# Kernel optimization log

Hardware: AMD Instinct MI355X
Metric: run time of the kernel (lower is better)

The kernel has to match this reference:

```python
import jax, jax.numpy as jnp
import numpy as np

D_MODEL = 1024
HEADS = 16
D_K = D_MODEL // HEADS
B, S = 2, 2048
NEG = -1000000000.0

def setup_inputs() -> dict:
    key = jax.random.key(0)
    ks = jax.random.split(key, 11)
    sc = 1.0 / np.sqrt(D_MODEL)
    inp = {
        'q': jax.random.normal(ks[0], (B, S, D_MODEL), jnp.float32),
        'k': jax.random.normal(ks[1], (B, S, D_MODEL), jnp.float32),
        'v': jax.random.normal(ks[2], (B, S, D_MODEL), jnp.float32),
        'mask': jnp.tril(jnp.ones((S, S), jnp.int32))[None, None],  # causal [1,1,S,S]
        'wq_w': jax.random.normal(ks[3], (D_MODEL, D_MODEL), jnp.float32) * sc,
        'wq_b': jax.random.normal(ks[4], (D_MODEL,), jnp.float32) * 0.02,
        'wk_w': jax.random.normal(ks[5], (D_MODEL, D_MODEL), jnp.float32) * sc,
        'wk_b': jax.random.normal(ks[6], (D_MODEL,), jnp.float32) * 0.02,
        'wv_w': jax.random.normal(ks[7], (D_MODEL, D_MODEL), jnp.float32) * sc,
        'wv_b': jax.random.normal(ks[8], (D_MODEL,), jnp.float32) * 0.02,
        'wo_w': jax.random.normal(ks[9], (D_MODEL, D_MODEL), jnp.float32) * sc,
        'wo_b': jax.random.normal(ks[10], (D_MODEL,), jnp.float32) * 0.02,
    }
    return inp

def reference(q, k, v, mask, wq_w, wq_b, wk_w, wk_b, wv_w, wv_b, wo_w, wo_b):
    b, s, _ = q.shape
    # projections (torch Linear: x @ W^T + b)
    Q = (q @ wq_w.T + wq_b).reshape(b, s, HEADS, D_K).transpose(0, 2, 1, 3)  # [B,H,S,Dk]
    K = (k @ wk_w.T + wk_b).reshape(b, s, HEADS, D_K).transpose(0, 2, 1, 3)
    V = (v @ wv_w.T + wv_b).reshape(b, s, HEADS, D_K).transpose(0, 2, 1, 3)
    scores = jnp.einsum('bhqd,bhkd->bhqk', Q, K) / jnp.sqrt(jnp.float32(D_K))
    scores = jnp.where(mask == 0, NEG, scores)
    p = jax.nn.softmax(scores, axis=-1)  # dropout=0.0 -> identity
    x = jnp.einsum('bhqk,bhkd->bhqd', p, V)
    x = x.transpose(0, 2, 1, 3).reshape(b, s, D_MODEL)
    return x @ wo_w.T + wo_b
```

## Files before the change

### kernel.cpp

```cpp
#include <hip/hip_runtime.h>

typedef unsigned short u16;
typedef __attribute__((ext_vector_type(8))) short bf16x8;
typedef __attribute__((ext_vector_type(4))) float f32x4;

#define SEQ 2048
#define DMODEL 1024

__device__ __forceinline__ u16 f2bf(float f) {
    union { float f; unsigned u; } x; x.f = f;
    unsigned r = x.u + 0x7fffu + ((x.u >> 16) & 1u);
    return (u16)(r >> 16);
}

__device__ __forceinline__ u16 f2bf_trunc(float f) {
    union { float f; unsigned u; } x; x.f = f;
    return (u16)(x.u >> 16);
}

__device__ __forceinline__ f32x4 mfma16(bf16x8 a, bf16x8 b, f32x4 c) {
    return __builtin_amdgcn_mfma_f32_16x16x32_bf16(a, b, c, 0, 0, 0);
}

__device__ __forceinline__ void gld16(const u16* g, u16* l) {
    __builtin_amdgcn_global_load_lds(
        (__attribute__((address_space(1))) const void*)g,
        (__attribute__((address_space(3))) void*)l, 16, 0, 0);
}

struct CvtArgs {
    const float* src[7];
    u16* dst[7];
    int n4[7];
};

__global__ __launch_bounds__(256) void cvt_kernel(CvtArgs a) {
    const int id = blockIdx.y;
    const int i = blockIdx.x * 256 + threadIdx.x;
    if (i >= a.n4[id]) return;
    float4 f = ((const float4*)a.src[id])[i];
    ushort4 u;
    u.x = f2bf(f.x); u.y = f2bf(f.y); u.z = f2bf(f.z); u.w = f2bf(f.w);
    ((ushort4*)a.dst[id])[i] = u;
}

__global__ __launch_bounds__(256) void gemm_qkv(
    const u16* __restrict__ Xq, const u16* __restrict__ Xk, const u16* __restrict__ Xv,
    const u16* __restrict__ Wq, const u16* __restrict__ Wk, const u16* __restrict__ Wv,
    const float* __restrict__ bq, const float* __restrict__ bk, const float* __restrict__ bv,
    u16* __restrict__ Qb, u16* __restrict__ Kb, u16* __restrict__ Vb)
{
    const int z = blockIdx.z;
    const u16* X = (z == 0) ? Xq : (z == 1) ? Xk : Xv;
    const u16* W = (z == 0) ? Wq : (z == 1) ? Wk : Wv;
    const float* bias = (z == 0) ? bq : (z == 1) ? bk : bv;

    __shared__ u16 As[128 * 32];
    __shared__ u16 Bs[128 * 32];

    const int tid = threadIdx.x;
    const int bm = blockIdx.y * 128, bn = blockIdx.x * 128;
    const int lane = tid & 63, w = tid >> 6;
    const int wm = (w >> 1) * 64, wn = (w & 1) * 64;
    const int r = lane & 15, qd = lane >> 4;

    const int cb0 = w * 64;
    const int cb1 = 256 + w * 64;
    const int c0 = cb0 + lane, c1 = cb1 + lane;
    const int r0 = c0 >> 2, o0 = (c0 & 3) * 8;
    const int r1 = c1 >> 2, o1 = (c1 & 3) * 8;

    f32x4 acc[4][4];
    #pragma unroll
    for (int i = 0; i < 4; ++i)
        #pragma unroll
        for (int j = 0; j < 4; ++j)
            acc[i][j] = (f32x4){0.f, 0.f, 0.f, 0.f};

    for (int kk = 0; kk < 1024; kk += 32) {
        __syncthreads();
        gld16(X + (size_t)(bm + r0) * 1024 + kk + o0, As + cb0 * 8);
        gld16(X + (size_t)(bm + r1) * 1024 + kk + o1, As + cb1 * 8);
        gld16(W + (size_t)(bn + r0) * 1024 + kk + o0, Bs + cb0 * 8);
        gld16(W + (size_t)(bn + r1) * 1024 + kk + o1, Bs + cb1 * 8);
        __syncthreads();

        bf16x8 aF[4], bF[4];
        #pragma unroll
        for (int i = 0; i < 4; ++i)
            aF[i] = *(const bf16x8*)(As + (wm + i * 16 + r) * 32 + qd * 8);
        #pragma unroll
        for (int j = 0; j < 4; ++j)
            bF[j] = *(const bf16x8*)(Bs + (wn + j * 16 + r) * 32 + qd * 8);
        #pragma unroll
        for (int i = 0; i < 4; ++i)
            #pragma unroll
            for (int j = 0; j < 4; ++j)
                acc[i][j] = mfma16(aF[i], bF[j], acc[i][j]);
    }

    const float scale = (z == 0) ? 0.125f : 1.0f;
    #pragma unroll
    for (int j = 0; j < 4; ++j) {
        const int n = bn + wn + j * 16 + r;
        const float bvl = bias[n];
        const int h = n >> 6, d = n & 63;
        #pragma unroll
        for (int i = 0; i < 4; ++i) {
            const int m0 = bm + wm + i * 16 + qd * 4;
            const int b_ = m0 >> 11, s0 = m0 & 2047;
            if (z == 0) {
                #pragma unroll
                for (int reg = 0; reg < 4; ++reg)
                    Qb[(size_t)(m0 + reg) * 1024 + n] = f2bf((acc[i][j][reg] + bvl) * scale);
            } else if (z == 1) {
                #pragma unroll
                for (int reg = 0; reg < 4; ++reg)
                    Kb[((size_t)(b_ * 16 + h) * SEQ + s0 + reg) * 64 + d] =
                        f2bf(acc[i][j][reg] + bvl);
            } else {
                ushort4 u;
                u.x = f2bf(acc[i][j][0] + bvl);
                u.y = f2bf(acc[i][j][1] + bvl);
                u.z = f2bf(acc[i][j][2] + bvl);
                u.w = f2bf(acc[i][j][3] + bvl);
                *(ushort4*)(Vb + ((size_t)(b_ * 16 + h) * 64 + d) * SEQ + s0) = u;
            }
        }
    }
}

__global__ __launch_bounds__(128, 3) void attn_kernel(
    const u16* __restrict__ Qb, const u16* __restrict__ Kb,
    const u16* __restrict__ Vb, u16* __restrict__ AO)
{
    __shared__ u16 Kst[2][4096];
    __shared__ u16 Vst[2][4096];
    __shared__ u16 Pst[2][16 * 72];

    const int bid = blockIdx.x;
    const int xcd = bid & 7;
    const int i2 = bid >> 3;
    const int bh = xcd + 8 * (i2 & 3);
    const int g  = 31 - (i2 >> 2);
    const int b_ = bh >> 4, h = bh & 15;

    const int tid = threadIdx.x;
    const int lane = tid & 63, w = tid >> 6;
    const int r = lane & 15, qd = lane >> 4;

    const u16* Kh = Kb + (size_t)bh * SEQ * 64;
    const u16* Vh = Vb + (size_t)bh * 64 * SEQ;
    u16* Pw = Pst[w];

    bf16x8 aQ[2][2];
    #pragma unroll
    for (int i = 0; i < 2; ++i) {
        const size_t qoff =
            (size_t)(b_ * SEQ + g * 64 + w * 32 + i * 16 + r) * DMODEL + h * 64;
        aQ[i][0] = *(const bf16x8*)(Qb + qoff + qd * 8);
        aQ[i][1] = *(const bf16x8*)(Qb + qoff + 32 + qd * 8);
    }

    bf16x8 ones;
    #pragma unroll
    for (int e = 0; e < 8; ++e) ones[e] = (short)0x3F80;

    f32x4 o[2][4];
    f32x4 l[2];
    #pragma unroll
    for (int i = 0; i < 2; ++i) {
        l[i] = (f32x4){0.f, 0.f, 0.f, 0.f};
        #pragma unroll
        for (int db = 0; db < 4; ++db) o[i][db] = (f32x4){0.f, 0.f, 0.f, 0.f};
    }

    auto stage = [&](int j, int buf) {
        if (w == 0) {
            const u16* Kt = Kh + (size_t)j * 64 * 64;
            #pragma unroll
            for (int s = 0; s < 8; ++s)
                gld16(Kt + ((s >> 1) * 16 + r) * 64 + (s & 1) * 32 + qd * 8,
                      &Kst[buf][s * 512]);
        } else {
            const u16* Vt = Vh + j * 64;
            #pragma unroll
            for (int s = 0; s < 8; ++s)
                gld16(Vt + (size_t)((s >> 1) * 16 + r) * SEQ + (s & 1) * 32 + qd * 8,
                      &Vst[buf][s * 512]);
        }
    };

    stage(0, 0);

    for (int j = 0; j <= g; ++j) {
        const int cur = j & 1;
        __syncthreads();
        if (j < g) stage(j + 1, 1 - cur);

        bf16x8 kf[4][2], vf[4][2];
        #pragma unroll
        for (int nb = 0; nb < 4; ++nb) {
            kf[nb][0] = *(const bf16x8*)(&Kst[cur][(nb * 2 + 0) * 512 + lane * 8]);
            kf[nb][1] = *(const bf16x8*)(&Kst[cur][(nb * 2 + 1) * 512 + lane * 8]);
        }
        #pragma unroll
        for (int db = 0; db < 4; ++db) {
            vf[db][0] = *(const bf16x8*)(&Vst[cur][(db * 2 + 0) * 512 + lane * 8]);
            vf[db][1] = *(const bf16x8*)(&Vst[cur][(db * 2 + 1) * 512 + lane * 8]);
        }

        #pragma unroll
        for (int i = 0; i < 2; ++i) {
            f32x4 sc[4];
            #pragma unroll
            for (int nb = 0; nb < 4; ++nb) {
                f32x4 s = (f32x4){0.f, 0.f, 0.f, 0.f};
                s = mfma16(kf[nb][0], aQ[i][0], s);
                s = mfma16(kf[nb][1], aQ[i][1], s);
                sc[nb] = s;
            }

            if (j == g) {
                const int rowr = w * 32 + i * 16 + r;
                #pragma unroll
                for (int nb = 0; nb < 4; ++nb)
                    #pragma unroll
                    for (int reg = 0; reg < 4; ++reg)
                        if (nb * 16 + qd * 4 + reg > rowr) sc[nb][reg] = -1e30f;
            }

            #pragma unroll
            for (int nb = 0; nb < 4; ++nb)
                #pragma unroll
                for (int reg = 0; reg < 4; ++reg)
                    sc[nb][reg] = exp2f(fmaf(sc[nb][reg], 1.4426950408889634f,
                                             -23.083120654223414f));

            #pragma unroll
            for (int nb = 0; nb < 4; ++nb) {
                ushort4 pk;
                pk.x = f2bf_trunc(sc[nb][0]);
                pk.y = f2bf_trunc(sc[nb][1]);
                pk.z = f2bf_trunc(sc[nb][2]);
                pk.w = f2bf_trunc(sc[nb][3]);
                *(ushort4*)(Pw + r * 72 + nb * 16 + qd * 4) = pk;
            }

            const bf16x8 aP0 = *(const bf16x8*)(Pw + r * 72 + qd * 8);
            const bf16x8 aP1 = *(const bf16x8*)(Pw + r * 72 + 32 + qd * 8);

            l[i] = mfma16(aP0, ones, l[i]);
            l[i] = mfma16(aP1, ones, l[i]);

            #pragma unroll
            for (int db = 0; db < 4; ++db) {
                o[i][db] = mfma16(aP0, vf[db][0], o[i][db]);
                o[i][db] = mfma16(aP1, vf[db][1], o[i][db]);
            }
        }
    }

    #pragma unroll
    for (int i = 0; i < 2; ++i)
        #pragma unroll
        for (int db = 0; db < 4; ++db)
            #pragma unroll
            for (int reg = 0; reg < 4; ++reg) {
                const int row = g * 64 + w * 32 + i * 16 + qd * 4 + reg;
                AO[(size_t)(b_ * SEQ + row) * DMODEL + h * 64 + db * 16 + r] =
                    f2bf(o[i][db][reg] / l[i][reg]);
            }
}

__global__ __launch_bounds__(256) void gemm_out(
    const u16* __restrict__ AO, const u16* __restrict__ W,
    const float* __restrict__ bias, float* __restrict__ out)
{
    __shared__ u16 As[128 * 32];
    __shared__ u16 Bs[128 * 32];

    const int tid = threadIdx.x;
    const int bm = blockIdx.y * 128, bn = blockIdx.x * 128;
    const int lane = tid & 63, w = tid >> 6;
    const int wm = (w >> 1) * 64, wn = (w & 1) * 64;
    const int r = lane & 15, qd = lane >> 4;

    const int cb0 = w * 64;
    const int cb1 = 256 + w * 64;
    const int c0 = cb0 + lane, c1 = cb1 + lane;
    const int r0 = c0 >> 2, o0 = (c0 & 3) * 8;
    const int r1 = c1 >> 2, o1 = (c1 & 3) * 8;

    f32x4 acc[4][4];
    #pragma unroll
    for (int i = 0; i < 4; ++i)
        #pragma unroll
        for (int j = 0; j < 4; ++j)
            acc[i][j] = (f32x4){0.f, 0.f, 0.f, 0.f};

    for (int kk = 0; kk < 1024; kk += 32) {
        __syncthreads();
        gld16(AO + (size_t)(bm + r0) * 1024 + kk + o0, As + cb0 * 8);
        gld16(AO + (size_t)(bm + r1) * 1024 + kk + o1, As + cb1 * 8);
        gld16(W + (size_t)(bn + r0) * 1024 + kk + o0, Bs + cb0 * 8);
        gld16(W + (size_t)(bn + r1) * 1024 + kk + o1, Bs + cb1 * 8);
        __syncthreads();

        bf16x8 aF[4], bF[4];
        #pragma unroll
        for (int i = 0; i < 4; ++i)
            aF[i] = *(const bf16x8*)(As + (wm + i * 16 + r) * 32 + qd * 8);
        #pragma unroll
        for (int j = 0; j < 4; ++j)
            bF[j] = *(const bf16x8*)(Bs + (wn + j * 16 + r) * 32 + qd * 8);
        #pragma unroll
        for (int i = 0; i < 4; ++i)
            #pragma unroll
            for (int j = 0; j < 4; ++j)
                acc[i][j] = mfma16(aF[i], bF[j], acc[i][j]);
    }

    #pragma unroll
    for (int j = 0; j < 4; ++j) {
        const int n = bn + wn + j * 16 + r;
        const float bvl = bias[n];
        #pragma unroll
        for (int i = 0; i < 4; ++i) {
            const int m0 = bm + wm + i * 16 + qd * 4;
            #pragma unroll
            for (int reg = 0; reg < 4; ++reg)
                out[(size_t)(m0 + reg) * 1024 + n] = acc[i][j][reg] + bvl;
        }
    }
}

extern "C" void kernel_launch(void* const* d_in, const int* in_sizes, int n_in,
                              void* d_out, int out_size, void* d_ws, size_t ws_size,
                              hipStream_t stream) {
    const float* q  = (const float*)d_in[0];
    const float* k  = (const float*)d_in[1];
    const float* v  = (const float*)d_in[2];
    const float* wq = (const float*)d_in[4];
    const float* bq = (const float*)d_in[5];
    const float* wk = (const float*)d_in[6];
    const float* bk = (const float*)d_in[7];
    const float* wv = (const float*)d_in[8];
    const float* bv = (const float*)d_in[9];
    const float* wo = (const float*)d_in[10];
    const float* bo = (const float*)d_in[11];
    float* out = (float*)d_out;

    u16* ws = (u16*)d_ws;
    u16* Xq = ws;
    u16* Xk = Xq + (size_t)4194304;
    u16* Xv = Xk + (size_t)4194304;
    u16* Wq = Xv + (size_t)4194304;
    u16* Wk = Wq + (size_t)1048576;
    u16* Wv = Wk + (size_t)1048576;
    u16* Wo = Wv + (size_t)1048576;
    u16* Qb = Wo + (size_t)1048576;
    u16* Kb = Qb + (size_t)4194304;
    u16* Vb = Kb + (size_t)4194304;
    u16* AO = Vb + (size_t)4194304;

    CvtArgs ca;
    ca.src[0] = q;  ca.dst[0] = Xq; ca.n4[0] = 1048576;
    ca.src[1] = k;  ca.dst[1] = Xk; ca.n4[1] = 1048576;
    ca.src[2] = v;  ca.dst[2] = Xv; ca.n4[2] = 1048576;
    ca.src[3] = wq; ca.dst[3] = Wq; ca.n4[3] = 262144;
    ca.src[4] = wk; ca.dst[4] = Wk; ca.n4[4] = 262144;
    ca.src[5] = wv; ca.dst[5] = Wv; ca.n4[5] = 262144;
    ca.src[6] = wo; ca.dst[6] = Wo; ca.n4[6] = 262144;

    cvt_kernel<<<dim3(4096, 7), 256, 0, stream>>>(ca);
    gemm_qkv<<<dim3(8, 32, 3), 256, 0, stream>>>(Xq, Xk, Xv, Wq, Wk, Wv,
                                                 bq, bk, bv, Qb, Kb, Vb);
    attn_kernel<<<dim3(1024), 128, 0, stream>>>(Qb, Kb, Vb, AO);
    gemm_out<<<dim3(8, 32), 256, 0, stream>>>(AO, Wo, bo, out);
}
```

Baseline: 262.6 us.

## Split causal attention KV range in two with a combine pass; XCD-remap GEMM blocks

Each attention query tile's key range is now split into two halves processed by separate blocks, doubling the grid to 2048 blocks. Each block writes unnormalized partial outputs and row sums to workspace, and a new attn_norm kernel adds the two partials and divides by the summed denominators. This targets load imbalance and low occupancy from causal tiles of very different lengths. The QKV and output GEMMs also switch to 1D grids with a mapping that keeps neighbouring M tiles on the same XCD, for better L2 reuse. The cost is an extra launch plus extra global traffic for the partial results.

Measured after the change: 255.5 us. 1.03x faster.

```diff
diff --git a/kernel.cpp b/kernel.cpp
--- a/kernel.cpp
+++ b/kernel.cpp
@@ -16,6 +16,11 @@
 __device__ __forceinline__ u16 f2bf_trunc(float f) {
     union { float f; unsigned u; } x; x.f = f;
     return (u16)(x.u >> 16);
+}
+
+__device__ __forceinline__ float bf2f(u16 v) {
+    union { unsigned u; float f; } x; x.u = ((unsigned)v) << 16;
+    return x.f;
 }
 
 __device__ __forceinline__ f32x4 mfma16(bf16x8 a, bf16x8 b, f32x4 c) {
@@ -50,7 +55,16 @@
     const float* __restrict__ bq, const float* __restrict__ bk, const float* __restrict__ bv,
     u16* __restrict__ Qb, u16* __restrict__ Kb, u16* __restrict__ Vb)
 {
-    const int z = blockIdx.z;
+    const int bid = blockIdx.x;
+    const int xcd = bid & 7;
+    const int li  = bid >> 3;
+    const int nb_ = li / 12;
+    const int mloc = li % 12;
+    const int gm  = xcd * 12 + mloc;
+    const int z   = gm >> 5;
+    const int bm  = (gm & 31) * 128;
+    const int bn  = nb_ * 128;
+
     const u16* X = (z == 0) ? Xq : (z == 1) ? Xk : Xv;
     const u16* W = (z == 0) ? Wq : (z == 1) ? Wk : Wv;
     const float* bias = (z == 0) ? bq : (z == 1) ? bk : bv;
@@ -59,7 +73,6 @@
     __shared__ u16 Bs[128 * 32];
 
     const int tid = threadIdx.x;
-    const int bm = blockIdx.y * 128, bn = blockIdx.x * 128;
     const int lane = tid & 63, w = tid >> 6;
     const int wm = (w >> 1) * 64, wn = (w & 1) * 64;
     const int r = lane & 15, qd = lane >> 4;
@@ -132,7 +145,7 @@
 
 __global__ __launch_bounds__(128, 3) void attn_kernel(
     const u16* __restrict__ Qb, const u16* __restrict__ Kb,
-    const u16* __restrict__ Vb, u16* __restrict__ AO)
+    const u16* __restrict__ Vb, u16* __restrict__ Op, float* __restrict__ Lp)
 {
     __shared__ u16 Kst[2][4096];
     __shared__ u16 Vst[2][4096];
@@ -142,8 +155,14 @@
     const int xcd = bid & 7;
     const int i2 = bid >> 3;
     const int bh = xcd + 8 * (i2 & 3);
-    const int g  = 31 - (i2 >> 2);
+    const int rest = i2 >> 2;
+    const int g = 31 - (rest >> 1);
+    const int half = rest & 1;
     const int b_ = bh >> 4, h = bh & 15;
+
+    const int h0 = (g + 1) >> 1;
+    const int j0 = half ? h0 : 0;
+    const int j1 = half ? (g + 1) : h0;
 
     const int tid = threadIdx.x;
     const int lane = tid & 63, w = tid >> 6;
@@ -191,12 +210,12 @@
         }
     };
 
-    stage(0, 0);
-
-    for (int j = 0; j <= g; ++j) {
+    if (j0 < j1) stage(j0, j0 & 1);
+
+    for (int j = j0; j < j1; ++j) {
         const int cur = j & 1;
         __syncthreads();
-        if (j < g) stage(j + 1, 1 - cur);
+        if (j + 1 < j1) stage(j + 1, 1 - cur);
 
         bf16x8 kf[4][2], vf[4][2];
         #pragma unroll
@@ -261,27 +280,65 @@
         }
     }
 
-    #pragma unroll
-    for (int i = 0; i < 2; ++i)
+    u16* Oh = Op + ((size_t)(half * 1024 + bh * 32 + g) * 4096);
+    float* Lh = Lp + (size_t)(half * 1024 + bh * 32 + g) * 64;
+    #pragma unroll
+    for (int i = 0; i < 2; ++i) {
         #pragma unroll
         for (int db = 0; db < 4; ++db)
             #pragma unroll
-            for (int reg = 0; reg < 4; ++reg) {
-                const int row = g * 64 + w * 32 + i * 16 + qd * 4 + reg;
-                AO[(size_t)(b_ * SEQ + row) * DMODEL + h * 64 + db * 16 + r] =
-                    f2bf(o[i][db][reg] / l[i][reg]);
-            }
+            for (int reg = 0; reg < 4; ++reg)
+                Oh[(w * 32 + i * 16 + qd * 4 + reg) * 64 + db * 16 + r] =
+                    f2bf(o[i][db][reg]);
+        if (r == 0) {
+            #pragma unroll
+            for (int reg = 0; reg < 4; ++reg)
+                Lh[w * 32 + i * 16 + qd * 4 + reg] = l[i][reg];
+        }
+    }
+}
+
+__global__ __launch_bounds__(256) void attn_norm(
+    const u16* __restrict__ Op, const float* __restrict__ Lp,
+    u16* __restrict__ AO)
+{
+    const int idx = blockIdx.x * 256 + threadIdx.x;
+    const int col8 = idx & 127;
+    const int row = idx >> 7;
+    const int h = col8 >> 3;
+    const int b_ = row >> 11, s = row & 2047;
+    const int g = s >> 6, r64 = s & 63;
+    const int bh = b_ * 16 + h;
+
+    const size_t pa = ((size_t)(bh * 32 + g) * 4096) + r64 * 64 + (col8 & 7) * 8;
+    const size_t pb = pa + (size_t)1024 * 4096;
+    const float la = Lp[(bh * 32 + g) * 64 + r64];
+    const float lb = Lp[(1024 + bh * 32 + g) * 64 + r64];
+    const float inv = 1.0f / (la + lb);
+
+    const bf16x8 a = *(const bf16x8*)(Op + pa);
+    const bf16x8 b = *(const bf16x8*)(Op + pb);
+    bf16x8 o;
+    #pragma unroll
+    for (int e = 0; e < 8; ++e)
+        o[e] = (short)f2bf((bf2f((u16)a[e]) + bf2f((u16)b[e])) * inv);
+    *(bf16x8*)(AO + (size_t)row * 1024 + col8 * 8) = o;
 }
 
 __global__ __launch_bounds__(256) void gemm_out(
     const u16* __restrict__ AO, const u16* __restrict__ W,
     const float* __restrict__ bias, float* __restrict__ out)
 {
+    const int bid = blockIdx.x;
+    const int xcd = bid & 7;
+    const int li = bid >> 3;
+    const int bn = (li >> 2) * 128;
+    const int bm = (xcd * 4 + (li & 3)) * 128;
+
     __shared__ u16 As[128 * 32];
     __shared__ u16 Bs[128 * 32];
 
     const int tid = threadIdx.x;
-    const int bm = blockIdx.y * 128, bn = blockIdx.x * 128;
     const int lane = tid & 63, w = tid >> 6;
     const int wm = (w >> 1) * 64, wn = (w & 1) * 64;
     const int r = lane & 15, qd = lane >> 4;
@@ -364,6 +421,9 @@
     u16* Vb = Kb + (size_t)4194304;
     u16* AO = Vb + (size_t)4194304;
 
+    u16* Op = ws;
+    float* Lp = (float*)(ws + (size_t)8388608);
+
     CvtArgs ca;
     ca.src[0] = q;  ca.dst[0] = Xq; ca.n4[0] = 1048576;
     ca.src[1] = k;  ca.dst[1] = Xk; ca.n4[1] = 1048576;
@@ -374,8 +434,9 @@
     ca.src[6] = wo; ca.dst[6] = Wo; ca.n4[6] = 262144;
 
     cvt_kernel<<<dim3(4096, 7), 256, 0, stream>>>(ca);
-    gemm_qkv<<<dim3(8, 32, 3), 256, 0, stream>>>(Xq, Xk, Xv, Wq, Wk, Wv,
-                                                 bq, bk, bv, Qb, Kb, Vb);
-    attn_kernel<<<dim3(1024), 128, 0, stream>>>(Qb, Kb, Vb, AO);
-    gemm_out<<<dim3(8, 32), 256, 0, stream>>>(AO, Wo, bo, out);
-}
+    gemm_qkv<<<dim3(768), 256, 0, stream>>>(Xq, Xk, Xv, Wq, Wk, Wv,
+                                            bq, bk, bv, Qb, Kb, Vb);
+    attn_kernel<<<dim3(2048), 128, 0, stream>>>(Qb, Kb, Vb, Op, Lp);
+    attn_norm<<<dim3(2048), 256, 0, stream>>>(Op, Lp, AO);
+    gemm_out<<<dim3(256), 256, 0, stream>>>(AO, Wo, bo, out);
+}
```
